# Kernel tuning notes

Measured on AMD Instinct MI355X. Metric: run time of the kernel, lower is better.

The kernel has to match this reference:

```python
import jax, jax.numpy as jnp
import numpy as np

N = 50000   # nodes
E = 800000  # edges
F = 128     # input features
W = 128     # hidden width
K = 5       # Chebyshev order


def setup_inputs() -> dict:
    key = jax.random.key(0)
    ks = jax.random.split(key, 12)
    x = jax.random.normal(ks[0], (N, F), jnp.float32)
    edge_index = jax.random.randint(ks[1], (2, E), 0, N, jnp.int32)
    def p(i, shape):
        return jax.random.normal(ks[i], shape, jnp.float32) * 0.05
    return {
        'x': x,
        'edge_index': edge_index,
        'W0': p(2, (K, F, W)), 'b0': p(3, (W,)),
        'W1': p(4, (K, W, W)), 'b1': p(5, (W,)),
        'W2': p(6, (K, W, W)), 'b2': p(7, (W,)),
        'Wl': p(8, (W, 1)),   'bl': p(9, (1,)),
    }


def _norm(edge_index):
    # PyG ChebConv norm with lambda_max=2.0, sym normalization:
    # Lhat = 2/lambda_max * (I - D^-1/2 A D^-1/2) - I  ->  diag 0, offdiag -d_r*d_c
    src, dst = edge_index[0], edge_index[1]
    ew = (src != dst).astype(jnp.float32)  # remove self loops
    deg = jax.ops.segment_sum(ew, src, num_segments=N)
    dinv = jnp.where(deg > 0, jax.lax.rsqrt(jnp.maximum(deg, 1.0)), 0.0)
    w = -ew * dinv[src] * dinv[dst]
    return src, dst, w


def _cheb_conv(h, Wk, b, src, dst, w):
    # Tx_0 = h; Tx_1 = Lhat h; Tx_k = 2 Lhat Tx_{k-1} - Tx_{k-2}
    def matvec(v):
        # gather from src, weight, scatter-add to dst: [E, C] message tensor
        return jax.ops.segment_sum(w[:, None] * v[src], dst, num_segments=N)
    Tx0 = h
    out = Tx0 @ Wk[0]
    Tx1 = matvec(Tx0)
    out = out + Tx1 @ Wk[1]
    for k in range(2, Wk.shape[0]):
        Tx2 = 2.0 * matvec(Tx1) - Tx0
        out = out + Tx2 @ Wk[k]
        Tx0, Tx1 = Tx1, Tx2
    return out + b


def reference(x, edge_index, W0, b0, W1, b1, W2, b2, Wl, bl):
    src, dst, w = _norm(edge_index)
    h = jax.nn.relu(_cheb_conv(x, W0, b0, src, dst, w))  # dropout = identity (eval)
    h = jax.nn.relu(_cheb_conv(h, W1, b1, src, dst, w))
    h = _cheb_conv(h, W2, b2, src, dst, w)
    return h @ Wl + bl  # [N, 1]
```

## Files before the change

kernel.cpp:

```cpp
#include <hip/hip_runtime.h>
#include <hip/hip_bf16.h>
#include <stdint.h>

#define N_NODES 50000
#define N_EDGES 800000
#define FEAT 128
#define CAP 64
#define PSLOT 16
#define NCVT 1600000

#define B_CONV_N 1563
#define B_EDGE_N 782
#define B_TOT 2509

typedef __attribute__((ext_vector_type(4))) float floatx4;
typedef __attribute__((ext_vector_type(8))) _Float16 half8;
typedef __attribute__((ext_vector_type(4))) _Float16 half4;
typedef __attribute__((ext_vector_type(4))) unsigned short ushortx4;
typedef __attribute__((ext_vector_type(4))) int intx4;

__device__ __forceinline__ float bf2f(unsigned short u) {
  union { unsigned u; float f; } v; v.u = ((unsigned)u) << 16; return v.f;
}
__device__ __forceinline__ unsigned short f2bf(float f) {
  union { float f; unsigned u; } v; v.f = f;
  unsigned r = v.u + 0x7fffu + ((v.u >> 16) & 1u);
  return (unsigned short)(r >> 16);
}
__device__ __forceinline__ unsigned pack_edge(float w, int s) {
  _Float16 h = (_Float16)w;
  unsigned short hb = __builtin_bit_cast(unsigned short, h);
  return ((unsigned)s << 16) | (unsigned)hb;
}
__device__ __forceinline__ float edge_w(unsigned e) {
  unsigned short hb = (unsigned short)(e & 0xFFFFu);
  return (float)__builtin_bit_cast(_Float16, hb);
}
__device__ __forceinline__ int edge_src(unsigned e) { return (int)(e >> 16); }

__device__ __forceinline__ half8 deq8(uint2 v, float sc) {
  half8 r;
  r[0] = (_Float16)(sc * (float)((int)(v.x & 0xFFu) - 128));
  r[1] = (_Float16)(sc * (float)((int)((v.x >> 8) & 0xFFu) - 128));
  r[2] = (_Float16)(sc * (float)((int)((v.x >> 16) & 0xFFu) - 128));
  r[3] = (_Float16)(sc * (float)((int)(v.x >> 24) - 128));
  r[4] = (_Float16)(sc * (float)((int)(v.y & 0xFFu) - 128));
  r[5] = (_Float16)(sc * (float)((int)((v.y >> 8) & 0xFFu) - 128));
  r[6] = (_Float16)(sc * (float)((int)((v.y >> 16) & 0xFFu) - 128));
  r[7] = (_Float16)(sc * (float)((int)(v.y >> 24) - 128));
  return r;
}

__global__ void k_pre1(const unsigned short* __restrict__ x,
                       const void* b0, const void* b1, const void* b2,
                       const void* wl, const void* bl,
                       float* __restrict__ pf, int* __restrict__ flag,
                       int* __restrict__ cnt8) {
  int tid = threadIdx.x;
  intx4 z = {0, 0, 0, 0};
  for (int i = blockIdx.x * 256 + tid; i < 112500; i += 64 * 256)
    ((intx4*)cnt8)[i] = z;
  if (blockIdx.x != 0) return;
  __shared__ int cnt_s;
  __shared__ int fl_s;
  if (tid == 0) cnt_s = 0;
  __syncthreads();
  int big = 0;
  for (int i = tid; i < 4096; i += 256) {
    unsigned short u = x[2 * i];
    int e = (u >> 7) & 0xFF;
    if (e >= 0xE0) big++;
  }
  atomicAdd(&cnt_s, big);
  __syncthreads();
  if (tid == 0) { fl_s = (cnt_s > 16) ? 1 : 0; flag[0] = fl_s; }
  __syncthreads();
  int fl = fl_s;
  for (int i = tid; i < 513; i += 256) {
    const void* src; int off;
    if (i < 128)      { src = b0; off = i; }
    else if (i < 256) { src = b1; off = i - 128; }
    else if (i < 384) { src = b2; off = i - 256; }
    else if (i < 512) { src = wl; off = i - 384; }
    else              { src = bl; off = 0; }
    pf[i] = fl ? ((const float*)src)[off] : bf2f(((const unsigned short*)src)[off]);
  }
}

__global__ void k_pre2(const void* __restrict__ xp,
                       const void* __restrict__ w0, const void* __restrict__ w1,
                       const void* __restrict__ w2,
                       const int* __restrict__ esrc, const int* __restrict__ edst,
                       _Float16* __restrict__ t0,
                       unsigned char* __restrict__ q0, float* __restrict__ s0,
                       _Float16* __restrict__ wt,
                       int* __restrict__ deg, int* __restrict__ cnt8,
                       unsigned short* __restrict__ edata16,
                       float* __restrict__ pf,
                       const int* __restrict__ flag) {
  int b = blockIdx.x, tid = threadIdx.x;
  if (b < 2346) {
    int g = b / 3, r = b - g * 3;
    if (r == 2) {
      int p = b & 7;
      int e0 = (g * 256 + tid) * 4;
      if (e0 >= N_EDGES) return;
      intx4 ss = __builtin_nontemporal_load((const intx4*)(esrc + e0));
      intx4 dd = __builtin_nontemporal_load((const intx4*)(edst + e0));
#pragma unroll
      for (int i = 0; i < 4; ++i) {
        int e = e0 + i;
        if (e >= N_EDGES) break;
        int s = ss[i], d = dd[i];
        if (s == d) continue;
        atomicAdd(&deg[s], 1);
        int pos = atomicAdd(&cnt8[p * N_NODES + d], 1);
        if (pos < PSLOT)
          edata16[(size_t)p * (N_NODES * PSLOT) + d * PSLOT + pos] = (unsigned short)s;
      }
      return;
    }
    int c = g * 2 + r;
    if (c >= B_CONV_N) return;
    int fl = flag[0];
    int base = c * 1024 + tid;
    floatx4 v[4];
    bool ok[4];
#pragma unroll
    for (int k = 0; k < 4; ++k) {
      int i = base + k * 256;
      ok[k] = i < NCVT;
      if (ok[k]) {
        if (fl) {
          v[k] = __builtin_nontemporal_load((const floatx4*)xp + i);
        } else {
          ushortx4 u = __builtin_nontemporal_load((const ushortx4*)xp + i);
          v[k].x = bf2f(u.x); v[k].y = bf2f(u.y); v[k].z = bf2f(u.z); v[k].w = bf2f(u.w);
        }
      }
    }
#pragma unroll
    for (int k = 0; k < 4; ++k) {
      if (!ok[k]) continue;
      int i = base + k * 256;
      half4 h;
      h[0] = (_Float16)v[k].x; h[1] = (_Float16)v[k].y;
      h[2] = (_Float16)v[k].z; h[3] = (_Float16)v[k].w;
      ((half4*)t0)[i] = h;
      float mx = fmaxf(fmaxf(fabsf(v[k].x), fabsf(v[k].y)), fmaxf(fabsf(v[k].z), fabsf(v[k].w)));
#pragma unroll
      for (int d = 1; d < 32; d <<= 1) mx = fmaxf(mx, __shfl_xor(mx, d));
      float inv = mx > 0.f ? 127.f / mx : 0.f;
      int qa = (int)rintf(v[k].x * inv) + 128;
      int qb = (int)rintf(v[k].y * inv) + 128;
      int qc = (int)rintf(v[k].z * inv) + 128;
      int qd = (int)rintf(v[k].w * inv) + 128;
      ((unsigned*)q0)[i] = (unsigned)qa | ((unsigned)qb << 8) | ((unsigned)qc << 16) | ((unsigned)qd << 24);
      if ((i & 31) == 0) s0[i >> 5] = mx > 0.f ? mx / 127.f : 0.f;
    }
  } else if (b < 2506) {
    int tb = (b - 2346) * 1024 + tid;
    int fl = flag[0];
#pragma unroll
    for (int k = 0; k < 4; ++k) {
      int t = tb + k * 256;
      int li = t >> 14;
      int rr = t & 16383;
      int n = rr >> 7, kk = rr & 127;
      int l = li / 5, kq = li - l * 5;
      const void* w = (l == 0) ? w0 : w1;
      int idx = kq * 16384 + kk * 128 + n;
      float vv = fl ? ((const float*)w)[idx] : bf2f(((const unsigned short*)w)[idx]);
      wt[t] = (_Float16)vv;
    }
  } else {
    int t = (b - 2506) * 256 + tid;
    if (t > 640) return;
    int fl = flag[0];
    if (t < 640) {
      int k = t >> 7, f = t & 127;
      float s = 0.f;
      const int base = (k << 14) + (f << 7);
      if (fl) {
        const float* w = (const float*)w2 + base;
#pragma unroll 8
        for (int q = 0; q < 128; ++q) s += w[q] * pf[384 + q];
      } else {
        const unsigned short* w = (const unsigned short*)w2 + base;
#pragma unroll 8
        for (int q = 0; q < 128; ++q) s += bf2f(w[q]) * pf[384 + q];
      }
      pf[520 + t] = s;
    } else {
      float s = 0.f;
      for (int q = 0; q < 128; ++q) s += pf[256 + q] * pf[384 + q];
      pf[1160] = s + pf[512];
    }
  }
}

__global__ __launch_bounds__(256) void k_wpack(const unsigned short* __restrict__ ed16,
                                               const int* __restrict__ cnt8,
                                               const int* __restrict__ deg,
                                               int* __restrict__ cnt,
                                               unsigned* __restrict__ edata) {
  int node = (blockIdx.x * 256 + threadIdx.x) >> 6;
  int lane = threadIdx.x & 63;
  if (node >= N_NODES) return;
  int c[8], off[8], tot = 0;
#pragma unroll
  for (int p = 0; p < 8; ++p) {
    int v = cnt8[p * N_NODES + node];
    if (v > PSLOT) v = PSLOT;
    c[p] = v; off[p] = tot; tot += v;
  }
  if (lane == 0) cnt[node] = tot > CAP ? CAP : tot;
  int dd = deg[node];
  float rd = dd > 0 ? rsqrtf((float)dd) : 0.f;
#pragma unroll
  for (int it = 0; it < 2; ++it) {
    int p = (lane >> 4) + it * 4;
    int s = lane & 15;
    if (s < c[p]) {
      int pos = off[p] + s;
      if (pos < CAP) {
        int sr = (int)ed16[(size_t)p * (N_NODES * PSLOT) + node * PSLOT + s];
        int ds = deg[sr];
        float w = (ds > 0 && dd > 0) ? -rsqrtf((float)ds) * rd : 0.f;
        edata[(node << 6) + pos] = pack_edge(w, sr);
      }
    }
  }
}

__global__ __launch_bounds__(256) void k_spmv(const unsigned* __restrict__ edata,
                                              const int* __restrict__ cnt,
                                              const unsigned char* __restrict__ Q,
                                              const float* __restrict__ S,
                                              const _Float16* __restrict__ Z,
                                              _Float16* __restrict__ Y,
                                              unsigned char* __restrict__ Qo,
                                              float* __restrict__ So,
                                              float alpha, int hasZ, int writeY) {
  int wave = threadIdx.x >> 6, lane = threadIdx.x & 63;
  int q = lane >> 4, l16 = lane & 15;
  int node = blockIdx.x * 16 + wave * 4 + q;
  if (node >= N_NODES) return;
  int n_e = cnt[node]; if (n_e > CAP) n_e = CAP;
  int base = node << 6;

  float acc[8];
#pragma unroll
  for (int f = 0; f < 8; ++f) acc[f] = 0.f;
  float wsum = 0.f;

  unsigned e0 = (0 < n_e) ? edata[base + 0] : 0u;
  unsigned e1 = (1 < n_e) ? edata[base + 1] : 0u;
  unsigned e2 = (2 < n_e) ? edata[base + 2] : 0u;
  unsigned e3 = (3 < n_e) ? edata[base + 3] : 0u;
  unsigned e4 = (4 < n_e) ? edata[base + 4] : 0u;
  unsigned e5 = (5 < n_e) ? edata[base + 5] : 0u;
  unsigned e6 = (6 < n_e) ? edata[base + 6] : 0u;
  unsigned e7 = (7 < n_e) ? edata[base + 7] : 0u;
  uint2 r0 = ((const uint2*)(Q + (size_t)edge_src(e0) * FEAT))[l16];
  uint2 r1 = ((const uint2*)(Q + (size_t)edge_src(e1) * FEAT))[l16];
  uint2 r2 = ((const uint2*)(Q + (size_t)edge_src(e2) * FEAT))[l16];
  uint2 r3 = ((const uint2*)(Q + (size_t)edge_src(e3) * FEAT))[l16];
  float s0 = S[edge_src(e0)], s1 = S[edge_src(e1)], s2 = S[edge_src(e2)], s3 = S[edge_src(e3)];

  for (int j = 0; j < n_e; j += 4) {
    float ws0 = edge_w(e0) * s0, ws1 = edge_w(e1) * s1;
    float ws2 = edge_w(e2) * s2, ws3 = edge_w(e3) * s3;
    uint2 c0 = r0, c1 = r1, c2 = r2, c3 = r3;
    e0 = e4; e1 = e5; e2 = e6; e3 = e7;
    e4 = (j + 8 < n_e) ? edata[base + j + 8] : 0u;
    e5 = (j + 9 < n_e) ? edata[base + j + 9] : 0u;
    e6 = (j + 10 < n_e) ? edata[base + j + 10] : 0u;
    e7 = (j + 11 < n_e) ? edata[base + j + 11] : 0u;
    r0 = ((const uint2*)(Q + (size_t)edge_src(e0) * FEAT))[l16];
    r1 = ((const uint2*)(Q + (size_t)edge_src(e1) * FEAT))[l16];
    r2 = ((const uint2*)(Q + (size_t)edge_src(e2) * FEAT))[l16];
    r3 = ((const uint2*)(Q + (size_t)edge_src(e3) * FEAT))[l16];
    s0 = S[edge_src(e0)]; s1 = S[edge_src(e1)]; s2 = S[edge_src(e2)]; s3 = S[edge_src(e3)];
#define DEC8(c, w)                                                        \
    acc[0] = fmaf(w, (float)(c.x & 0xFFu), acc[0]);                       \
    acc[1] = fmaf(w, (float)((c.x >> 8) & 0xFFu), acc[1]);                \
    acc[2] = fmaf(w, (float)((c.x >> 16) & 0xFFu), acc[2]);               \
    acc[3] = fmaf(w, (float)(c.x >> 24), acc[3]);                         \
    acc[4] = fmaf(w, (float)(c.y & 0xFFu), acc[4]);                       \
    acc[5] = fmaf(w, (float)((c.y >> 8) & 0xFFu), acc[5]);                \
    acc[6] = fmaf(w, (float)((c.y >> 16) & 0xFFu), acc[6]);               \
    acc[7] = fmaf(w, (float)(c.y >> 24), acc[7]);
    DEC8(c0, ws0) DEC8(c1, ws1) DEC8(c2, ws2) DEC8(c3, ws3)
#undef DEC8
    wsum += (ws0 + ws1) + (ws2 + ws3);
  }
  float rx[8];
  float b128 = 128.f * wsum;
  if (hasZ) {
    half8 z = ((const half8*)(Z + (size_t)node * FEAT))[l16];
#pragma unroll
    for (int f = 0; f < 8; ++f) rx[f] = fmaf(alpha, acc[f] - b128, -(float)z[f]);
  } else {
#pragma unroll
    for (int f = 0; f < 8; ++f) rx[f] = alpha * (acc[f] - b128);
  }
  if (writeY) {
    half8 res;
#pragma unroll
    for (int f = 0; f < 8; ++f) res[f] = (_Float16)rx[f];
    ((half8*)(Y + (size_t)node * FEAT))[l16] = res;
  }
  float mx = 0.f;
#pragma unroll
  for (int f = 0; f < 8; ++f) mx = fmaxf(mx, fabsf(rx[f]));
#pragma unroll
  for (int o = 1; o < 16; o <<= 1) mx = fmaxf(mx, __shfl_xor(mx, o));
  float inv = mx > 0.f ? 127.f / mx : 0.f;
  int qb[8];
#pragma unroll
  for (int f = 0; f < 8; ++f) qb[f] = (int)rintf(rx[f] * inv) + 128;
  uint2 p;
  p.x = (unsigned)qb[0] | ((unsigned)qb[1] << 8) | ((unsigned)qb[2] << 16) | ((unsigned)qb[3] << 24);
  p.y = (unsigned)qb[4] | ((unsigned)qb[5] << 8) | ((unsigned)qb[6] << 16) | ((unsigned)qb[7] << 24);
  ((uint2*)(Qo + (size_t)node * FEAT))[l16] = p;
  if (l16 == 0) So[node] = mx > 0.f ? mx / 127.f : 0.f;
}

__global__ __launch_bounds__(256) void k_smv(const unsigned* __restrict__ edata,
                                             const int* __restrict__ cnt,
                                             const float* __restrict__ h,
                                             const float* __restrict__ b,
                                             const float* __restrict__ bprev,
                                             float cL, float* __restrict__ y,
                                             int is_out, void* __restrict__ outp,
                                             const int* __restrict__ flag,
                                             const float* __restrict__ cptr) {
  int wave = threadIdx.x >> 6, lane = threadIdx.x & 63;
  int q = lane >> 4, l16 = lane & 15;
  int node = blockIdx.x * 16 + wave * 4 + q;
  if (node >= N_NODES) return;
  int n_e = cnt[node]; if (n_e > CAP) n_e = CAP;
  int base = node << 6;
  float s = 0.f;
  for (int j = l16; j < n_e; j += 16) {
    unsigned e = edata[base + j];
    s = fmaf(edge_w(e), b[edge_src(e)], s);
  }
#pragma unroll
  for (int o = 1; o < 16; o <<= 1) s += __shfl_xor(s, o);
  if (l16 == 0) {
    float r = fmaf(cL, s, h[node]) - (bprev ? bprev[node] : 0.f);
    if (!is_out) {
      y[node] = r;
    } else {
      r += cptr[0];
      if (flag[0]) ((float*)outp)[node] = r;
      else ((unsigned short*)outp)[node] = f2bf(r);
    }
  }
}

__global__ __launch_bounds__(256) void k_gemm(const unsigned char* __restrict__ qa0, const unsigned char* __restrict__ qa1,
                                              const unsigned char* __restrict__ qa2, const unsigned char* __restrict__ qa3,
                                              const unsigned char* __restrict__ qa4,
                                              const float* __restrict__ sa0, const float* __restrict__ sa1,
                                              const float* __restrict__ sa2, const float* __restrict__ sa3,
                                              const float* __restrict__ sa4,
                                              const _Float16* __restrict__ wt,
                                              const float* __restrict__ bias,
                                              _Float16* __restrict__ dst, int mode,
                                              const float* __restrict__ v0,
                                              float* __restrict__ hout,
                                              unsigned char* __restrict__ q8out,
                                              float* __restrict__ scout) {
  __shared__ _Float16 lb[128 * 136];
  const unsigned char* qp[5] = {qa0, qa1, qa2, qa3, qa4};
  const float* sp[5] = {sa0, sa1, sa2, sa3, sa4};
  int tid = threadIdx.x, wave = tid >> 6, lane = tid & 63;
  int quad = lane >> 4, l16 = lane & 15;
  int m0 = blockIdx.x * 128;
  floatx4 acc[2][8];
#pragma unroll
  for (int s = 0; s < 2; ++s)
#pragma unroll
    for (int j = 0; j < 8; ++j) acc[s][j] = (floatx4){0.f, 0.f, 0.f, 0.f};
  int arow[2];
  bool aval[2];
#pragma unroll
  for (int s = 0; s < 2; ++s) {
    arow[s] = m0 + wave * 32 + s * 16 + l16;
    aval[s] = arow[s] < N_NODES;
  }

#pragma unroll
  for (int k = 0; k < 5; ++k) {
    __syncthreads();
    {
      int n = tid >> 1, half = tid & 1;
      const uint4* spw = (const uint4*)(wt + k * 16384 + n * 128 + half * 64);
      uint4* dq = (uint4*)(lb + n * 136 + half * 64);
#pragma unroll
      for (int i = 0; i < 8; ++i) dq[i] = spw[i];
    }
    __syncthreads();
    const unsigned char* Aq = qp[k];
    float sk[2];
#pragma unroll
    for (int s = 0; s < 2; ++s) sk[s] = aval[s] ? sp[k][arow[s]] : 0.f;
#pragma unroll
    for (int ki = 0; ki < 4; ++ki) {
      half8 af[2];
#pragma unroll
      for (int s = 0; s < 2; ++s) {
        uint2 qv = aval[s]
          ? *((const uint2*)(Aq + (size_t)arow[s] * FEAT + ki * 32 + quad * 8))
          : make_uint2(0x80808080u, 0x80808080u);
        af[s] = deq8(qv, sk[s]);
      }
#pragma unroll
      for (int j = 0; j < 8; ++j) {
        half8 bf = *((const half8*)(lb + (j * 16 + l16) * 136 + ki * 32 + quad * 8));
        acc[0][j] = __builtin_amdgcn_mfma_f32_16x16x32_f16(af[0], bf, acc[0][j], 0, 0, 0);
        acc[1][j] = __builtin_amdgcn_mfma_f32_16x16x32_f16(af[1], bf, acc[1][j], 0, 0, 0);
      }
    }
  }
#pragma unroll
  for (int s = 0; s < 2; ++s) {
    int rbase = m0 + wave * 32 + s * 16 + quad * 4;
    if (mode == 0) {
      float mx[4] = {0.f, 0.f, 0.f, 0.f};
#pragma unroll
      for (int j = 0; j < 8; ++j) {
        int col = j * 16 + l16;
        float b = bias[col];
#pragma unroll
        for (int r = 0; r < 4; ++r) {
          int m = rbase + r;
          float v = fmaxf(acc[s][j][r] + b, 0.f);
          if (m < N_NODES) dst[(size_t)m * FEAT + col] = (_Float16)v;
          mx[r] = fmaxf(mx[r], v);
        }
      }
#pragma unroll
      for (int o = 1; o < 16; o <<= 1) {
#pragma unroll
        for (int r = 0; r < 4; ++r) mx[r] = fmaxf(mx[r], __shfl_xor(mx[r], o));
      }
      float inv[4];
#pragma unroll
      for (int r = 0; r < 4; ++r) inv[r] = mx[r] > 0.f ? 127.f / mx[r] : 0.f;
      if (l16 == 0) {
#pragma unroll
        for (int r = 0; r < 4; ++r) {
          int m = rbase + r;
          if (m < N_NODES) scout[m] = mx[r] > 0.f ? mx[r] / 127.f : 0.f;
        }
      }
#pragma unroll
      for (int j = 0; j < 8; ++j) {
        int col = j * 16 + l16;
        float b = bias[col];
#pragma unroll
        for (int r = 0; r < 4; ++r) {
          int m = rbase + r;
          if (m < N_NODES) {
            float v = fmaxf(acc[s][j][r] + b, 0.f);
            int qv = (int)rintf(v * inv[r]) + 128;
            q8out[(size_t)m * FEAT + col] = (unsigned char)qv;
          }
        }
      }
    } else {
      float p[5][4];
#pragma unroll
      for (int k = 0; k < 5; ++k)
#pragma unroll
        for (int r = 0; r < 4; ++r) p[k][r] = 0.f;
#pragma unroll
      for (int j = 0; j < 8; ++j) {
        int col = j * 16 + l16;
        float b = bias[col];
        float vv[5];
#pragma unroll
        for (int k = 0; k < 5; ++k) vv[k] = v0[k * 128 + col];
#pragma unroll
        for (int r = 0; r < 4; ++r) {
          float val = fmaxf(acc[s][j][r] + b, 0.f);
#pragma unroll
          for (int k = 0; k < 5; ++k) p[k][r] = fmaf(val, vv[k], p[k][r]);
        }
      }
#pragma unroll
      for (int o = 1; o < 16; o <<= 1) {
#pragma unroll
        for (int k = 0; k < 5; ++k)
#pragma unroll
          for (int r = 0; r < 4; ++r) p[k][r] += __shfl_xor(p[k][r], o);
      }
      if (l16 == 0) {
#pragma unroll
        for (int r = 0; r < 4; ++r) {
          int m = rbase + r;
          if (m < N_NODES) {
#pragma unroll
            for (int k = 0; k < 5; ++k) hout[k * N_NODES + m] = p[k][r];
          }
        }
      }
    }
  }
}

extern "C" void kernel_launch(void* const* d_in, const int* in_sizes, int n_in,
                              void* d_out, int out_size, void* d_ws, size_t ws_size,
                              hipStream_t stream) {
  const void* x  = d_in[0];
  const int* ei  = (const int*)d_in[1];
  const void* w0 = d_in[2];
  const void* b0 = d_in[3];
  const void* w1 = d_in[4];
  const void* b1 = d_in[5];
  const void* w2 = d_in[6];
  const void* b2 = d_in[7];
  const void* wl = d_in[8];
  const void* bl = d_in[9];
  const int* src = ei;
  const int* dst = ei + N_EDGES;

  char* ws = (char*)d_ws;
  size_t off = 0;
  auto alloc = [&](size_t bytes) -> char* {
    char* p = ws + off;
    off += (bytes + 255) & ~(size_t)255;
    return p;
  };
  _Float16* T[3];
  for (int i = 0; i < 3; ++i) T[i] = (_Float16*)alloc(sizeof(_Float16) * N_NODES * FEAT);
  unsigned char* Q[5];
  for (int i = 0; i < 5; ++i) Q[i] = (unsigned char*)alloc((size_t)N_NODES * FEAT);
  float* S[5];
  for (int i = 0; i < 5; ++i) S[i] = (float*)alloc(sizeof(float) * N_NODES);
  unsigned* edata = (unsigned*)alloc(sizeof(unsigned) * N_NODES * CAP);
  unsigned short* edata16 = (unsigned short*)alloc(sizeof(unsigned short) * 8 * N_NODES * PSLOT);
  int* cnt8 = (int*)alloc(sizeof(int) * N_NODES * 9);
  int* deg = cnt8 + 8 * N_NODES;
  int* cnt = (int*)alloc(sizeof(int) * N_NODES);
  _Float16* wt = (_Float16*)alloc(sizeof(_Float16) * 163840);
  float* pf = (float*)alloc(sizeof(float) * 1536);
  float* hbuf = (float*)alloc(sizeof(float) * 5 * N_NODES);
  float* bbuf = (float*)alloc(sizeof(float) * 3 * N_NODES);
  int* flag = (int*)alloc(sizeof(int));

  k_pre1<<<64, 256, 0, stream>>>((const unsigned short*)x, b0, b1, b2, wl, bl, pf, flag, cnt8);
  k_pre2<<<B_TOT, 256, 0, stream>>>(x, w0, w1, w2, src, dst, T[0], Q[0], S[0], wt,
                                    deg, cnt8, edata16, pf, flag);
  k_wpack<<<(N_NODES * 64 + 255) / 256, 256, 0, stream>>>(edata16, cnt8, deg, cnt, edata);

  int nblk_spmv = (N_NODES + 15) / 16;
  int nblk_gemm = (N_NODES + 127) / 128;
  const float* v = pf + 520;
  const float* cc = pf + 1160;

  for (int l = 0; l < 2; ++l) {
    k_spmv<<<nblk_spmv, 256, 0, stream>>>(edata, cnt, Q[0], S[0], nullptr, T[1], Q[1], S[1], 1.f, 0, 1);
    k_spmv<<<nblk_spmv, 256, 0, stream>>>(edata, cnt, Q[1], S[1], T[0], T[2], Q[2], S[2], 2.f, 1, 1);
    k_spmv<<<nblk_spmv, 256, 0, stream>>>(edata, cnt, Q[2], S[2], T[1], nullptr, Q[3], S[3], 2.f, 1, 0);
    k_spmv<<<nblk_spmv, 256, 0, stream>>>(edata, cnt, Q[3], S[3], T[2], nullptr, Q[4], S[4], 2.f, 1, 0);
    k_gemm<<<nblk_gemm, 256, 0, stream>>>(Q[0], Q[1], Q[2], Q[3], Q[4],
                                          S[0], S[1], S[2], S[3], S[4],
                                          wt + l * 5 * 16384, pf + l * 128, T[0],
                                          l, v, hbuf, Q[0], S[0]);
  }
  float* h0 = hbuf;
  float* h1 = hbuf + N_NODES;
  float* h2 = hbuf + 2 * N_NODES;
  float* h3 = hbuf + 3 * N_NODES;
  float* h4 = hbuf + 4 * N_NODES;
  float* b3 = bbuf;
  float* b2c = bbuf + N_NODES;
  float* b1c = bbuf + 2 * N_NODES;
  k_smv<<<nblk_spmv, 256, 0, stream>>>(edata, cnt, h3, h4, nullptr, 2.f, b3, 0, nullptr, flag, nullptr);
  k_smv<<<nblk_spmv, 256, 0, stream>>>(edata, cnt, h2, b3, h4, 2.f, b2c, 0, nullptr, flag, nullptr);
  k_smv<<<nblk_spmv, 256, 0, stream>>>(edata, cnt, h1, b2c, b3, 2.f, b1c, 0, nullptr, flag, nullptr);
  k_smv<<<nblk_spmv, 256, 0, stream>>>(edata, cnt, h0, b1c, b2c, 1.f, nullptr, 1, d_out, flag, cc);
}
```

Measured before the change: 454.2 us.

## Bucket edges by destination block and deepen SpMV gather prefetch

Graph construction stops scattering into eight per-partition, per-node slot arrays. Edges are now appended as packed (dst,src) pairs into 1024 coarse buckets of 49 nodes each, and a new per-bucket kernel sorts them into per-node lists in shared memory before computing weights. This cuts the atomic-counter footprint and the scattered writes in preprocessing. Separately, the SpMV inner loop now processes 8 edges per iteration and prefetches 16 edge words ahead, instead of 4 and 8, to keep more gathers in flight at the cost of more registers; bucket overflow beyond 1152 edges silently drops edges.

```diff
diff --git a/kernel.cpp b/kernel.cpp
--- a/kernel.cpp
+++ b/kernel.cpp
@@ -6,11 +6,13 @@
 #define N_EDGES 800000
 #define FEAT 128
 #define CAP 64
-#define PSLOT 16
 #define NCVT 1600000
 
+#define NBKT 1024
+#define BNODES 49
+#define SLOTA 1152
+
 #define B_CONV_N 1563
-#define B_EDGE_N 782
 #define B_TOT 2509
 
 typedef __attribute__((ext_vector_type(4))) float floatx4;
@@ -55,11 +57,11 @@
                        const void* b0, const void* b1, const void* b2,
                        const void* wl, const void* bl,
                        float* __restrict__ pf, int* __restrict__ flag,
-                       int* __restrict__ cnt8) {
+                       int* __restrict__ degcnt) {
   int tid = threadIdx.x;
   intx4 z = {0, 0, 0, 0};
-  for (int i = blockIdx.x * 256 + tid; i < 112500; i += 64 * 256)
-    ((intx4*)cnt8)[i] = z;
+  for (int i = blockIdx.x * 256 + tid; i < 12800; i += 64 * 256)
+    ((intx4*)degcnt)[i] = z;
   if (blockIdx.x != 0) return;
   __shared__ int cnt_s;
   __shared__ int fl_s;
@@ -94,29 +96,27 @@
                        _Float16* __restrict__ t0,
                        unsigned char* __restrict__ q0, float* __restrict__ s0,
                        _Float16* __restrict__ wt,
-                       int* __restrict__ deg, int* __restrict__ cnt8,
-                       unsigned short* __restrict__ edata16,
+                       int* __restrict__ deg, int* __restrict__ cntA,
+                       unsigned* __restrict__ pairs,
                        float* __restrict__ pf,
                        const int* __restrict__ flag) {
   int b = blockIdx.x, tid = threadIdx.x;
   if (b < 2346) {
     int g = b / 3, r = b - g * 3;
     if (r == 2) {
-      int p = b & 7;
       int e0 = (g * 256 + tid) * 4;
       if (e0 >= N_EDGES) return;
       intx4 ss = __builtin_nontemporal_load((const intx4*)(esrc + e0));
       intx4 dd = __builtin_nontemporal_load((const intx4*)(edst + e0));
 #pragma unroll
       for (int i = 0; i < 4; ++i) {
-        int e = e0 + i;
-        if (e >= N_EDGES) break;
         int s = ss[i], d = dd[i];
         if (s == d) continue;
         atomicAdd(&deg[s], 1);
-        int pos = atomicAdd(&cnt8[p * N_NODES + d], 1);
-        if (pos < PSLOT)
-          edata16[(size_t)p * (N_NODES * PSLOT) + d * PSLOT + pos] = (unsigned short)s;
+        int bk = d / BNODES;
+        int pos = atomicAdd(&cntA[bk], 1);
+        if (pos < SLOTA)
+          pairs[bk * SLOTA + pos] = ((unsigned)d << 16) | (unsigned)s;
       }
       return;
     }
@@ -199,36 +199,37 @@
   }
 }
 
-__global__ __launch_bounds__(256) void k_wpack(const unsigned short* __restrict__ ed16,
-                                               const int* __restrict__ cnt8,
+__global__ __launch_bounds__(256) void k_edgeB(const unsigned* __restrict__ pairs,
+                                               const int* __restrict__ cntA,
                                                const int* __restrict__ deg,
                                                int* __restrict__ cnt,
                                                unsigned* __restrict__ edata) {
-  int node = (blockIdx.x * 256 + threadIdx.x) >> 6;
-  int lane = threadIdx.x & 63;
-  if (node >= N_NODES) return;
-  int c[8], off[8], tot = 0;
-#pragma unroll
-  for (int p = 0; p < 8; ++p) {
-    int v = cnt8[p * N_NODES + node];
-    if (v > PSLOT) v = PSLOT;
-    c[p] = v; off[p] = tot; tot += v;
-  }
-  if (lane == 0) cnt[node] = tot > CAP ? CAP : tot;
-  int dd = deg[node];
-  float rd = dd > 0 ? rsqrtf((float)dd) : 0.f;
-#pragma unroll
-  for (int it = 0; it < 2; ++it) {
-    int p = (lane >> 4) + it * 4;
-    int s = lane & 15;
-    if (s < c[p]) {
-      int pos = off[p] + s;
-      if (pos < CAP) {
-        int sr = (int)ed16[(size_t)p * (N_NODES * PSLOT) + node * PSLOT + s];
-        int ds = deg[sr];
-        float w = (ds > 0 && dd > 0) ? -rsqrtf((float)ds) * rd : 0.f;
-        edata[(node << 6) + pos] = pack_edge(w, sr);
-      }
+  __shared__ unsigned short lsrc[BNODES * CAP];
+  __shared__ int lcnt[BNODES];
+  int tid = threadIdx.x, b = blockIdx.x;
+  if (tid < BNODES) lcnt[tid] = 0;
+  __syncthreads();
+  int n0 = b * BNODES;
+  int nb = cntA[b]; if (nb > SLOTA) nb = SLOTA;
+  for (int i = tid; i < nb; i += 256) {
+    unsigned pr = pairs[b * SLOTA + i];
+    int d = (int)(pr >> 16), s = (int)(pr & 0xFFFFu);
+    int ln = d - n0;
+    int pos = atomicAdd(&lcnt[ln], 1);
+    if (pos < CAP) lsrc[ln * CAP + pos] = (unsigned short)s;
+  }
+  __syncthreads();
+  for (int slot = tid; slot < BNODES * CAP; slot += 256) {
+    int ln = slot >> 6, s = slot & 63;
+    int node = n0 + ln;
+    if (node >= N_NODES) continue;
+    int c = lcnt[ln]; if (c > CAP) c = CAP;
+    if (s == 0) cnt[node] = c;
+    if (s < c) {
+      int sr = (int)lsrc[slot];
+      int ds = deg[sr], dd = deg[node];
+      float w = (ds > 0 && dd > 0) ? -rsqrtf((float)ds) * rsqrtf((float)dd) : 0.f;
+      edata[(node << 6) + s] = pack_edge(w, sr);
     }
   }
 }
@@ -254,46 +255,44 @@
   for (int f = 0; f < 8; ++f) acc[f] = 0.f;
   float wsum = 0.f;
 
-  unsigned e0 = (0 < n_e) ? edata[base + 0] : 0u;
-  unsigned e1 = (1 < n_e) ? edata[base + 1] : 0u;
-  unsigned e2 = (2 < n_e) ? edata[base + 2] : 0u;
-  unsigned e3 = (3 < n_e) ? edata[base + 3] : 0u;
-  unsigned e4 = (4 < n_e) ? edata[base + 4] : 0u;
-  unsigned e5 = (5 < n_e) ? edata[base + 5] : 0u;
-  unsigned e6 = (6 < n_e) ? edata[base + 6] : 0u;
-  unsigned e7 = (7 < n_e) ? edata[base + 7] : 0u;
-  uint2 r0 = ((const uint2*)(Q + (size_t)edge_src(e0) * FEAT))[l16];
-  uint2 r1 = ((const uint2*)(Q + (size_t)edge_src(e1) * FEAT))[l16];
-  uint2 r2 = ((const uint2*)(Q + (size_t)edge_src(e2) * FEAT))[l16];
-  uint2 r3 = ((const uint2*)(Q + (size_t)edge_src(e3) * FEAT))[l16];
-  float s0 = S[edge_src(e0)], s1 = S[edge_src(e1)], s2 = S[edge_src(e2)], s3 = S[edge_src(e3)];
-
-  for (int j = 0; j < n_e; j += 4) {
-    float ws0 = edge_w(e0) * s0, ws1 = edge_w(e1) * s1;
-    float ws2 = edge_w(e2) * s2, ws3 = edge_w(e3) * s3;
-    uint2 c0 = r0, c1 = r1, c2 = r2, c3 = r3;
-    e0 = e4; e1 = e5; e2 = e6; e3 = e7;
-    e4 = (j + 8 < n_e) ? edata[base + j + 8] : 0u;
-    e5 = (j + 9 < n_e) ? edata[base + j + 9] : 0u;
-    e6 = (j + 10 < n_e) ? edata[base + j + 10] : 0u;
-    e7 = (j + 11 < n_e) ? edata[base + j + 11] : 0u;
-    r0 = ((const uint2*)(Q + (size_t)edge_src(e0) * FEAT))[l16];
-    r1 = ((const uint2*)(Q + (size_t)edge_src(e1) * FEAT))[l16];
-    r2 = ((const uint2*)(Q + (size_t)edge_src(e2) * FEAT))[l16];
-    r3 = ((const uint2*)(Q + (size_t)edge_src(e3) * FEAT))[l16];
-    s0 = S[edge_src(e0)]; s1 = S[edge_src(e1)]; s2 = S[edge_src(e2)]; s3 = S[edge_src(e3)];
-#define DEC8(c, w)                                                        \
-    acc[0] = fmaf(w, (float)(c.x & 0xFFu), acc[0]);                       \
-    acc[1] = fmaf(w, (float)((c.x >> 8) & 0xFFu), acc[1]);                \
-    acc[2] = fmaf(w, (float)((c.x >> 16) & 0xFFu), acc[2]);               \
-    acc[3] = fmaf(w, (float)(c.x >> 24), acc[3]);                         \
-    acc[4] = fmaf(w, (float)(c.y & 0xFFu), acc[4]);                       \
-    acc[5] = fmaf(w, (float)((c.y >> 8) & 0xFFu), acc[5]);                \
-    acc[6] = fmaf(w, (float)((c.y >> 16) & 0xFFu), acc[6]);               \
-    acc[7] = fmaf(w, (float)(c.y >> 24), acc[7]);
-    DEC8(c0, ws0) DEC8(c1, ws1) DEC8(c2, ws2) DEC8(c3, ws3)
+  unsigned e[16];
+#pragma unroll
+  for (int i = 0; i < 16; ++i) e[i] = (i < n_e) ? edata[base + i] : 0u;
+  uint2 r[8];
+  float sv[8];
+#pragma unroll
+  for (int i = 0; i < 8; ++i) {
+    r[i] = ((const uint2*)(Q + (size_t)edge_src(e[i]) * FEAT))[l16];
+    sv[i] = S[edge_src(e[i])];
+  }
+
+  for (int j = 0; j < n_e; j += 8) {
+    float ws[8];
+    uint2 c[8];
+#pragma unroll
+    for (int i = 0; i < 8; ++i) { ws[i] = edge_w(e[i]) * sv[i]; c[i] = r[i]; }
+#pragma unroll
+    for (int i = 0; i < 8; ++i) e[i] = e[i + 8];
+#pragma unroll
+    for (int i = 0; i < 8; ++i)
+      e[i + 8] = (j + 16 + i < n_e) ? edata[base + j + 16 + i] : 0u;
+#pragma unroll
+    for (int i = 0; i < 8; ++i) {
+      r[i] = ((const uint2*)(Q + (size_t)edge_src(e[i]) * FEAT))[l16];
+      sv[i] = S[edge_src(e[i])];
+    }
+#define DEC8(cc, w)                                                       \
+    acc[0] = fmaf(w, (float)(cc.x & 0xFFu), acc[0]);                      \
+    acc[1] = fmaf(w, (float)((cc.x >> 8) & 0xFFu), acc[1]);               \
+    acc[2] = fmaf(w, (float)((cc.x >> 16) & 0xFFu), acc[2]);              \
+    acc[3] = fmaf(w, (float)(cc.x >> 24), acc[3]);                        \
+    acc[4] = fmaf(w, (float)(cc.y & 0xFFu), acc[4]);                      \
+    acc[5] = fmaf(w, (float)((cc.y >> 8) & 0xFFu), acc[5]);               \
+    acc[6] = fmaf(w, (float)((cc.y >> 16) & 0xFFu), acc[6]);              \
+    acc[7] = fmaf(w, (float)(cc.y >> 24), acc[7]);
+#pragma unroll
+    for (int i = 0; i < 8; ++i) { DEC8(c[i], ws[i]) wsum += ws[i]; }
 #undef DEC8
-    wsum += (ws0 + ws1) + (ws2 + ws3);
   }
   float rx[8];
   float b128 = 128.f * wsum;
@@ -543,9 +542,10 @@
   float* S[5];
   for (int i = 0; i < 5; ++i) S[i] = (float*)alloc(sizeof(float) * N_NODES);
   unsigned* edata = (unsigned*)alloc(sizeof(unsigned) * N_NODES * CAP);
-  unsigned short* edata16 = (unsigned short*)alloc(sizeof(unsigned short) * 8 * N_NODES * PSLOT);
-  int* cnt8 = (int*)alloc(sizeof(int) * N_NODES * 9);
-  int* deg = cnt8 + 8 * N_NODES;
+  unsigned* pairs = (unsigned*)alloc(sizeof(unsigned) * NBKT * SLOTA);
+  int* degcnt = (int*)alloc(sizeof(int) * 51200);
+  int* deg = degcnt;
+  int* cntA = degcnt + N_NODES;
   int* cnt = (int*)alloc(sizeof(int) * N_NODES);
   _Float16* wt = (_Float16*)alloc(sizeof(_Float16) * 163840);
   float* pf = (float*)alloc(sizeof(float) * 1536);
@@ -553,10 +553,10 @@
   float* bbuf = (float*)alloc(sizeof(float) * 3 * N_NODES);
   int* flag = (int*)alloc(sizeof(int));
 
-  k_pre1<<<64, 256, 0, stream>>>((const unsigned short*)x, b0, b1, b2, wl, bl, pf, flag, cnt8);
+  k_pre1<<<64, 256, 0, stream>>>((const unsigned short*)x, b0, b1, b2, wl, bl, pf, flag, degcnt);
   k_pre2<<<B_TOT, 256, 0, stream>>>(x, w0, w1, w2, src, dst, T[0], Q[0], S[0], wt,
-                                    deg, cnt8, edata16, pf, flag);
-  k_wpack<<<(N_NODES * 64 + 255) / 256, 256, 0, stream>>>(edata16, cnt8, deg, cnt, edata);
+                                    deg, cntA, pairs, pf, flag);
+  k_edgeB<<<NBKT, 256, 0, stream>>>(pairs, cntA, deg, cnt, edata);
 
   int nblk_spmv = (N_NODES + 15) / 16;
   int nblk_gemm = (N_NODES + 127) / 128;
```

After: 580.8 us. 1.28x slower.
